# Kernel tuning notes

Measured on AMD Instinct MI355X. Metric: run time of the kernel, lower is better.

Reference implementation:

```python
import jax, jax.numpy as jnp
import numpy as np

KS = (7, 7)
ST = (3, 3)
PD = (3, 3)
DIM = 512
HID = 1960  # 40 * 49, divisible by kernel_shape


def _patch_flat_idx(out_h, out_w):
    kh, kw = KS; sh, sw = ST; ph, pw = PD
    oh = (out_h + 2 * ph - kh) // sh + 1
    ow = (out_w + 2 * pw - kw) // sw + 1
    Wp = out_w + 2 * pw
    iy = jnp.arange(kh)[:, None, None, None] + (jnp.arange(oh) * sh)[None, None, :, None]
    ix = jnp.arange(kw)[None, :, None, None] + (jnp.arange(ow) * sw)[None, None, None, :]
    # (kh, kw, oh, ow) flat index into padded image
    return (iy * Wp + ix), oh, ow


def fold(patches, out_h, out_w):
    # patches: (B, C*kh*kw, L) -> (B, C, out_h, out_w), overlap-add like F.fold
    kh, kw = KS; ph, pw = PD
    idx, oh, ow = _patch_flat_idx(out_h, out_w)
    B, CK, L = patches.shape
    C = CK // (kh * kw)
    Hp, Wp = out_h + 2 * ph, out_w + 2 * pw
    p = patches.reshape(B, C, kh, kw, oh, ow)
    out = jnp.zeros((B, C, Hp * Wp), patches.dtype)
    out = out.at[:, :, idx.reshape(-1)].add(p.reshape(B, C, -1))
    return out.reshape(B, C, Hp, Wp)[:, :, ph:ph + out_h, pw:pw + out_w]


def unfold(img, out_h, out_w):
    # img: (B, C, H, W) -> (B, C*kh*kw, L), like F.unfold
    kh, kw = KS; ph, pw = PD
    idx, oh, ow = _patch_flat_idx(out_h, out_w)
    B, C = img.shape[:2]
    imgp = jnp.pad(img, ((0, 0), (0, 0), (ph, ph), (pw, pw)))
    flat = imgp.reshape(B, C, -1)
    g = flat[:, :, idx.reshape(-1)].reshape(B, C, kh, kw, oh, ow)
    return g.reshape(B, C * kh * kw, oh * ow)


def setup_inputs() -> dict:
    key = jax.random.key(0)
    k1, k2, k3, k4, k5 = jax.random.split(key, 5)
    x = jax.random.normal(k1, (2, 5760, DIM), dtype=jnp.float32)
    W1 = jax.random.normal(k2, (HID, DIM), dtype=jnp.float32) * 0.02
    b1 = jax.random.normal(k3, (HID,), dtype=jnp.float32) * 0.02
    W2 = jax.random.normal(k4, (DIM, HID), dtype=jnp.float32) * 0.02
    b2 = jax.random.normal(k5, (DIM,), dtype=jnp.float32) * 0.02
    return {"x": x, "W1": W1, "b1": b1, "W2": W2, "b2": b2, "out_h": 60, "out_w": 108}


def reference(x, W1, b1, W2, b2, out_h, out_w):
    kh, kw = KS; sh, sw = ST; ph, pw = PD
    oh = (out_h + 2 * ph - kh) // sh + 1
    ow = (out_w + 2 * pw - kw) // sw + 1
    n_vecs = oh * ow
    h = jnp.einsum('bnd,hd->bnh', x, W1) + b1          # (b, n, HID)
    b_, n, c = h.shape
    p = h.reshape(-1, n_vecs, c).transpose(0, 2, 1)     # (B', c, L)
    folded = fold(p, out_h, out_w)                      # (B', c//49, H, W)
    ones = jnp.ones((p.shape[0], kh * kw, n_vecs), h.dtype)
    norm = fold(ones, out_h, out_w)                     # (B', 1, H, W)
    y = unfold(folded / norm, out_h, out_w)             # (B', c, L)
    y = y.transpose(0, 2, 1).reshape(b_, n, c)
    out = jnp.einsum('bnh,dh->bnd', jax.nn.gelu(y, approximate=False), W2) + b2
    return out
```

## Files before the change

### kernel.cpp

```cpp
#include <hip/hip_runtime.h>
#include <cmath>

#define M_ROWS   11520
#define DIM      512
#define HID      1960
#define HIDP     2048
#define KP2      1984
#define OH       20
#define OW       36
#define LVEC     720
#define NCH      40
#define BPRIME   16
#define HP       66
#define WP       114

typedef unsigned short u16;
typedef __bf16 bf16x8 __attribute__((ext_vector_type(8)));
typedef float  f32x4  __attribute__((ext_vector_type(4)));

__device__ __forceinline__ u16 f2bf(float f) {
    unsigned u = __float_as_uint(f);
    u += 0x7fffu + ((u >> 16) & 1u);
    return (u16)(u >> 16);
}
__device__ __forceinline__ float bf2f(u16 h) {
    return __uint_as_float(((unsigned)h) << 16);
}

__device__ __forceinline__ void gload_lds16(const void* g, void* l) {
    __builtin_amdgcn_global_load_lds(
        (const __attribute__((address_space(1))) void*)g,
        (__attribute__((address_space(3))) void*)l, 16, 0, 0);
}

#define CVT_XB   5760
#define CVT_W1B  1024
#define CVT_W2B  1024
#define CVT_Z    270
__global__ __launch_bounds__(256) void cvt_all(const float* __restrict__ x,
                                               const float* __restrict__ W1,
                                               const float* __restrict__ W2,
                                               u16* __restrict__ xb,
                                               u16* __restrict__ W1b,
                                               u16* __restrict__ W2b,
                                               u16* __restrict__ g2) {
    const int b = blockIdx.x;
    const int tid = threadIdx.x;
    ushort4 o;
    if (b < CVT_XB) {
        int i = (b * 256 + tid) * 4;
        float4 v = *(const float4*)(x + i);
        o.x = f2bf(v.x); o.y = f2bf(v.y); o.z = f2bf(v.z); o.w = f2bf(v.w);
        *(ushort4*)(xb + i) = o;
    } else if (b < CVT_XB + CVT_W1B) {
        int i = ((b - CVT_XB) * 256 + tid) * 4;
        if (i < HID * DIM) {
            float4 v = *(const float4*)(W1 + i);
            o.x = f2bf(v.x); o.y = f2bf(v.y); o.z = f2bf(v.z); o.w = f2bf(v.w);
        } else {
            o.x = o.y = o.z = o.w = 0;
        }
        *(ushort4*)(W1b + i) = o;
    } else if (b < CVT_XB + CVT_W1B + CVT_W2B) {
        int i = ((b - CVT_XB - CVT_W1B) * 256 + tid) * 4;
        int d = i / HIDP, c = i - d * HIDP;
        if (c < HID) {
            float4 v = *(const float4*)(W2 + (size_t)d * HID + c);
            o.x = f2bf(v.x); o.y = f2bf(v.y); o.z = f2bf(v.z); o.w = f2bf(v.w);
        } else {
            o.x = o.y = o.z = o.w = 0;
        }
        *(ushort4*)(W2b + i) = o;
    } else {
        int i = ((b - CVT_XB - CVT_W1B - CVT_W2B) * 256 + tid) * 4;
        int row = i / 24, c = i - row * 24;
        o.x = o.y = o.z = o.w = 0;
        *(ushort4*)(g2 + (size_t)row * HIDP + HID + c) = o;
    }
}

template <int OUT_BF16, int BN>
__global__ __launch_bounds__(512) void gemm_bt(const u16* __restrict__ A,
                                               const u16* __restrict__ B,
                                               const float* __restrict__ bias,
                                               int biasN, void* __restrict__ Cout,
                                               int N, int K, int ldk) {
    constexpr int WN = BN / 2;
    constexpr int NU = WN / 16;
    constexpr int BCH = BN * 8;

    __shared__ u16 sA[128 * 64];
    __shared__ u16 sB[BN * 64];

    const int tid  = threadIdx.x;
    const int ntn  = N / BN;
    const int NB   = gridDim.x;
    const int v    = (blockIdx.x & 7) * (NB >> 3) + (blockIdx.x >> 3);
    const int bm   = v / ntn;
    const int bn   = v - bm * ntn;
    const int lane = tid & 63;
    const int wv   = tid >> 6;
    const int wm   = (wv >> 1) * 32;
    const int wn   = (wv & 1) * WN;
    const int r    = lane & 15;
    const int quad = lane >> 4;

    const size_t Arow0 = (size_t)bm * 128 * ldk;
    const size_t Brow0 = (size_t)bn * BN * ldk;

    f32x4 acc[2][NU] = {};

    for (int kt = 0; kt < K; kt += 64) {
        __syncthreads();
#pragma unroll
        for (int i = 0; i < 2; i++) {
            int e   = i * 512 + tid;
            int row = e >> 3;
            int cp  = e & 7;
            int cg  = cp ^ (row & 7);
            gload_lds16(A + Arow0 + (size_t)row * ldk + kt + cg * 8, (char*)sA + e * 16);
        }
#pragma unroll
        for (int i = 0; i < BCH / 512; i++) {
            int e   = i * 512 + tid;
            int row = e >> 3;
            int cp  = e & 7;
            int cg  = cp ^ (row & 7);
            gload_lds16(B + Brow0 + (size_t)row * ldk + kt + cg * 8, (char*)sB + e * 16);
        }
        __syncthreads();
#pragma unroll
        for (int kk = 0; kk < 2; kk++) {
            bf16x8 af[2], bg[NU];
#pragma unroll
            for (int t = 0; t < 2; t++) {
                int row = wm + t * 16 + r;
                int c   = (kk * 4 + quad) ^ (row & 7);
                af[t] = *(const bf16x8*)(sA + row * 64 + c * 8);
            }
#pragma unroll
            for (int u = 0; u < NU; u++) {
                int row = wn + u * 16 + r;
                int c   = (kk * 4 + quad) ^ (row & 7);
                bg[u] = *(const bf16x8*)(sB + row * 64 + c * 8);
            }
#pragma unroll
            for (int t = 0; t < 2; t++)
#pragma unroll
                for (int u = 0; u < NU; u++)
                    acc[t][u] = __builtin_amdgcn_mfma_f32_16x16x32_bf16(
                        af[t], bg[u], acc[t][u], 0, 0, 0);
        }
    }

    const int gm0 = bm * 128 + wm;
    const int gn0 = bn * BN + wn;
#pragma unroll
    for (int u = 0; u < NU; u++) {
        int gn = gn0 + u * 16 + r;
        float bv = (gn < biasN) ? bias[gn] : 0.0f;
#pragma unroll
        for (int t = 0; t < 2; t++) {
            int gm = gm0 + t * 16 + quad * 4;
#pragma unroll
            for (int q = 0; q < 4; q++) {
                float v2 = acc[t][u][q] + bv;
                if (OUT_BF16)
                    ((u16*)Cout)[(size_t)(gm + q) * N + gn] = f2bf(v2);
                else
                    ((float*)Cout)[(size_t)(gm + q) * N + gn] = v2;
            }
        }
    }
}

__global__ __launch_bounds__(512) void mid_fused(const u16* __restrict__ hg,
                                                 u16* __restrict__ g2) {
    __shared__ u16 sh[12 * 20 * 56];
    __shared__ u16 sG[34 * 58];

    const int b   = blockIdx.x;
    const int bp  = b / (NCH * 4);
    const int rr  = b - bp * (NCH * 4);
    const int ch  = rr >> 2;
    const int s   = (rr >> 1) & 1;
    const int xh  = rr & 1;
    const int o0  = s * 10;
    const int lo  = s * 8;
    const int ox0 = xh * 16;
    const int n0  = bp * LVEC;
    const int c0  = ch * 49;
    const int c0f = c0 & ~7;
    const int koff = c0 & 7;
    const int tid = threadIdx.x;

    {
        const char* hb = (const char*)(hg + (size_t)(n0 + lo * 36 + ox0) * HIDP + c0f);
        for (int t = tid; t < 12 * 20 * 7; t += 512) {
            int r   = (int)(((unsigned)t * 74899u) >> 19);
            int c   = t - r * 7;
            int loy = (int)(((unsigned)r * 3277u) >> 16);
            int oxl = r - 20 * loy;
            gload_lds16(hb + (size_t)(loy * 36 + oxl) * (HIDP * 2) + c * 16,
                        (char*)sh + t * 16);
        }
    }
    __syncthreads();

    const int pxl = tid & 63;
    const int rg  = tid >> 6;
    if (pxl < 58) {
        const int  pxg  = pxl + 54 * xh;
        const bool pxin = (pxg >= 3) && (pxg <= 110);
        const int  kx0  = pxg % 3;
        int  ct[3];
        bool vx[3];
        int  cx = 0;
#pragma unroll
        for (int dx = 0; dx < 3; dx++) {
            int kx = kx0 + 3 * dx, rx = pxg - kx;
            bool ok = pxin && (kx <= 6) && (rx >= 0) && (rx <= 105);
            vx[dx] = ok;
            ct[dx] = ok ? ((rx / 3) - ox0) * 56 + kx : 0;
            cx += ok ? 1 : 0;
        }
        const float fcx = (cx == 3) ? (1.0f / 3.0f) : ((cx == 2) ? 0.5f : 1.0f);

        for (int pr = rg; pr < 34; pr += 8) {
            int py = 3 * o0 + pr;
            float val = 0.0f;
            if (pxin && py >= 3 && py <= 62) {
                int ky0 = py % 3;
                float sum = 0.0f;
                int cy = 0;
#pragma unroll
                for (int dy = 0; dy < 3; dy++) {
                    int ky = ky0 + 3 * dy, ry = py - ky;
                    if (ky <= 6 && ry >= 0 && ry <= 57) {
                        int rt = (ry / 3 - lo) * (20 * 56) + ky * 7 + koff;
                        cy++;
                        float v0 = bf2f(sh[rt + ct[0]]);
                        float v1 = bf2f(sh[rt + ct[1]]);
                        float v2 = bf2f(sh[rt + ct[2]]);
                        sum += vx[0] ? v0 : 0.0f;
                        sum += vx[1] ? v1 : 0.0f;
                        sum += vx[2] ? v2 : 0.0f;
                    }
                }
                float fcy = (cy == 3) ? (1.0f / 3.0f) : ((cy == 2) ? 0.5f : 1.0f);
                float m = sum * fcx * fcy;
                val = 0.5f * m * (1.0f + erff(m * 0.70710678118654752f));
            }
            sG[pr * 58 + pxl] = f2bf(val);
        }
    }
    __syncthreads();

    {
        u16* g2row = g2 + (size_t)(n0 + o0 * 36 + 18 * xh) * HIDP + c0;
        for (int j = tid; j < 10 * 18 * 49; j += 512) {
            int l2 = (int)(((unsigned)j * 42800u) >> 21);
            int k  = j - l2 * 49;
            int oy = (int)(((unsigned)l2 * 57u) >> 10);
            int ox = l2 - 18 * oy;
            int ky = (int)(((unsigned)k * 37u) >> 8);
            int kx = k - 7 * ky;
            g2row[(size_t)(oy * 36 + ox) * HIDP + k] =
                sG[(3 * oy + ky) * 58 + 3 * ox + kx];
        }
    }
}

extern "C" void kernel_launch(void* const* d_in, const int* in_sizes, int n_in,
                              void* d_out, int out_size, void* d_ws, size_t ws_size,
                              hipStream_t stream) {
    (void)in_sizes; (void)n_in; (void)out_size; (void)ws_size;
    const float* x  = (const float*)d_in[0];
    const float* W1 = (const float*)d_in[1];
    const float* b1 = (const float*)d_in[2];
    const float* W2 = (const float*)d_in[3];
    const float* b2 = (const float*)d_in[4];
    float* out = (float*)d_out;

    char* ws = (char*)d_ws;
    u16* xb  = (u16*)(ws);
    u16* W1b = (u16*)(ws + 11796480);
    u16* W2b = (u16*)(ws + 13893632);
    u16* hg  = (u16*)(ws + 15990784);
    u16* g2  = (u16*)(ws + 63176704);

    cvt_all<<<CVT_XB + CVT_W1B + CVT_W2B + CVT_Z, 256, 0, stream>>>(
        x, W1, W2, xb, W1b, W2b, g2);

    gemm_bt<1, 128><<<(M_ROWS / 128) * (HIDP / 128), 512, 0, stream>>>(
        xb, W1b, b1, HID, (void*)hg, HIDP, DIM, DIM);

    mid_fused<<<BPRIME * NCH * 4, 512, 0, stream>>>(hg, g2);

    gemm_bt<0, 64><<<(M_ROWS / 128) * (DIM / 64), 512, 0, stream>>>(
        g2, W2b, b2, DIM, (void*)out, DIM, KP2, HIDP);
}
```

Baseline: 186.8 us.

## Specialize GEMM kernels, use 1024-thread GEMM1 with LDS-staged coalesced output

Result: slower. 193.6 us (+3.6%).

```diff
diff --git a/kernel.cpp b/kernel.cpp
--- a/kernel.cpp
+++ b/kernel.cpp
@@ -11,12 +11,11 @@
 #define LVEC     720
 #define NCH      40
 #define BPRIME   16
-#define HP       66
-#define WP       114
 
 typedef unsigned short u16;
 typedef __bf16 bf16x8 __attribute__((ext_vector_type(8)));
 typedef float  f32x4  __attribute__((ext_vector_type(4)));
+typedef unsigned short u16x8 __attribute__((ext_vector_type(8)));
 
 __device__ __forceinline__ u16 f2bf(float f) {
     unsigned u = __float_as_uint(f);
@@ -79,97 +78,162 @@
     }
 }
 
-template <int OUT_BF16, int BN>
-__global__ __launch_bounds__(512) void gemm_bt(const u16* __restrict__ A,
-                                               const u16* __restrict__ B,
-                                               const float* __restrict__ bias,
-                                               int biasN, void* __restrict__ Cout,
-                                               int N, int K, int ldk) {
-    constexpr int WN = BN / 2;
-    constexpr int NU = WN / 16;
-    constexpr int BCH = BN * 8;
-
-    __shared__ u16 sA[128 * 64];
-    __shared__ u16 sB[BN * 64];
+__global__ __launch_bounds__(1024, 8) void gemm1_k(const u16* __restrict__ A,
+                                                   const u16* __restrict__ B,
+                                                   const float* __restrict__ bias,
+                                                   u16* __restrict__ C) {
+    __shared__ u16 smem[128 * 136];
+    u16* sA = smem;
+    u16* sB = smem + 128 * 64;
 
     const int tid  = threadIdx.x;
-    const int ntn  = N / BN;
     const int NB   = gridDim.x;
     const int v    = (blockIdx.x & 7) * (NB >> 3) + (blockIdx.x >> 3);
-    const int bm   = v / ntn;
-    const int bn   = v - bm * ntn;
+    const int bm   = v >> 4;
+    const int bn   = v & 15;
+    const int lane = tid & 63;
+    const int wv   = tid >> 6;
+    const int wm   = (wv >> 2) * 32;
+    const int wn   = (wv & 3) * 32;
+    const int r    = lane & 15;
+    const int quad = lane >> 4;
+
+    const size_t Arow0 = (size_t)bm * 128 * DIM;
+    const size_t Brow0 = (size_t)bn * 128 * DIM;
+
+    const int srow = tid >> 3;
+    const int scg  = (tid & 7) ^ (srow & 7);
+
+    f32x4 acc[2][2] = {};
+
+    for (int kt = 0; kt < DIM; kt += 64) {
+        __syncthreads();
+        gload_lds16(A + Arow0 + (size_t)srow * DIM + kt + scg * 8, (char*)sA + tid * 16);
+        gload_lds16(B + Brow0 + (size_t)srow * DIM + kt + scg * 8, (char*)sB + tid * 16);
+        __syncthreads();
+#pragma unroll
+        for (int kk = 0; kk < 2; kk++) {
+            bf16x8 af[2], bg[2];
+#pragma unroll
+            for (int m = 0; m < 2; m++) {
+                int row = wm + m * 16 + r;
+                int c   = (kk * 4 + quad) ^ (row & 7);
+                af[m] = *(const bf16x8*)(sA + row * 64 + c * 8);
+            }
+#pragma unroll
+            for (int u = 0; u < 2; u++) {
+                int row = wn + u * 16 + r;
+                int c   = (kk * 4 + quad) ^ (row & 7);
+                bg[u] = *(const bf16x8*)(sB + row * 64 + c * 8);
+            }
+#pragma unroll
+            for (int m = 0; m < 2; m++)
+#pragma unroll
+                for (int u = 0; u < 2; u++)
+                    acc[m][u] = __builtin_amdgcn_mfma_f32_16x16x32_bf16(
+                        af[m], bg[u], acc[m][u], 0, 0, 0);
+        }
+    }
+
+    __syncthreads();
+    const int gn0 = bn * 128;
+#pragma unroll
+    for (int u = 0; u < 2; u++) {
+        int gnl = wn + u * 16 + r;
+        int gng = gn0 + gnl;
+        float bv = (gng < HID) ? bias[gng] : 0.0f;
+#pragma unroll
+        for (int m = 0; m < 2; m++) {
+            int gml = wm + m * 16 + quad * 4;
+#pragma unroll
+            for (int q = 0; q < 4; q++)
+                smem[(gml + q) * 136 + gnl] = f2bf(acc[m][u][q] + bv);
+        }
+    }
+    __syncthreads();
+    const int row = tid >> 3;
+    const int seg = tid & 7;
+    const u16* src = smem + row * 136 + seg * 16;
+    u16* dst = C + (size_t)(bm * 128 + row) * HIDP + gn0 + seg * 16;
+    *(u16x8*)dst       = *(const u16x8*)src;
+    *(u16x8*)(dst + 8) = *(const u16x8*)(src + 8);
+}
+
+__global__ __launch_bounds__(512, 8) void gemm2_k(const u16* __restrict__ A,
+                                                  const u16* __restrict__ B,
+                                                  const float* __restrict__ bias,
+                                                  float* __restrict__ C) {
+    __shared__ u16 sA[128 * 64];
+    __shared__ u16 sB[64 * 64];
+
+    const int tid  = threadIdx.x;
+    const int NB   = gridDim.x;
+    const int v    = (blockIdx.x & 7) * (NB >> 3) + (blockIdx.x >> 3);
+    const int bm   = v >> 3;
+    const int bn   = v & 7;
     const int lane = tid & 63;
     const int wv   = tid >> 6;
     const int wm   = (wv >> 1) * 32;
-    const int wn   = (wv & 1) * WN;
+    const int wn   = (wv & 1) * 32;
     const int r    = lane & 15;
     const int quad = lane >> 4;
 
-    const size_t Arow0 = (size_t)bm * 128 * ldk;
-    const size_t Brow0 = (size_t)bn * BN * ldk;
-
-    f32x4 acc[2][NU] = {};
-
-    for (int kt = 0; kt < K; kt += 64) {
+    const size_t Arow0 = (size_t)bm * 128 * HIDP;
+    const size_t Brow0 = (size_t)bn * 64 * HIDP;
+
+    f32x4 acc[2][2] = {};
+
+    for (int kt = 0; kt < KP2; kt += 64) {
         __syncthreads();
 #pragma unroll
         for (int i = 0; i < 2; i++) {
             int e   = i * 512 + tid;
             int row = e >> 3;
-            int cp  = e & 7;
-            int cg  = cp ^ (row & 7);
-            gload_lds16(A + Arow0 + (size_t)row * ldk + kt + cg * 8, (char*)sA + e * 16);
-        }
-#pragma unroll
-        for (int i = 0; i < BCH / 512; i++) {
-            int e   = i * 512 + tid;
-            int row = e >> 3;
-            int cp  = e & 7;
-            int cg  = cp ^ (row & 7);
-            gload_lds16(B + Brow0 + (size_t)row * ldk + kt + cg * 8, (char*)sB + e * 16);
+            int cg  = (e & 7) ^ (row & 7);
+            gload_lds16(A + Arow0 + (size_t)row * HIDP + kt + cg * 8, (char*)sA + e * 16);
+        }
+        {
+            int row = tid >> 3;
+            int cg  = (tid & 7) ^ (row & 7);
+            gload_lds16(B + Brow0 + (size_t)row * HIDP + kt + cg * 8, (char*)sB + tid * 16);
         }
         __syncthreads();
 #pragma unroll
         for (int kk = 0; kk < 2; kk++) {
-            bf16x8 af[2], bg[NU];
-#pragma unroll
-            for (int t = 0; t < 2; t++) {
-                int row = wm + t * 16 + r;
+            bf16x8 af[2], bg[2];
+#pragma unroll
+            for (int m = 0; m < 2; m++) {
+                int row = wm + m * 16 + r;
                 int c   = (kk * 4 + quad) ^ (row & 7);
-                af[t] = *(const bf16x8*)(sA + row * 64 + c * 8);
-            }
-#pragma unroll
-            for (int u = 0; u < NU; u++) {
+                af[m] = *(const bf16x8*)(sA + row * 64 + c * 8);
+            }
+#pragma unroll
+            for (int u = 0; u < 2; u++) {
                 int row = wn + u * 16 + r;
                 int c   = (kk * 4 + quad) ^ (row & 7);
                 bg[u] = *(const bf16x8*)(sB + row * 64 + c * 8);
             }
 #pragma unroll
-            for (int t = 0; t < 2; t++)
-#pragma unroll
-                for (int u = 0; u < NU; u++)
-                    acc[t][u] = __builtin_amdgcn_mfma_f32_16x16x32_bf16(
-                        af[t], bg[u], acc[t][u], 0, 0, 0);
+            for (int m = 0; m < 2; m++)
+#pragma unroll
+                for (int u = 0; u < 2; u++)
+                    acc[m][u] = __builtin_amdgcn_mfma_f32_16x16x32_bf16(
+                        af[m], bg[u], acc[m][u], 0, 0, 0);
         }
     }
 
     const int gm0 = bm * 128 + wm;
-    const int gn0 = bn * BN + wn;
-#pragma unroll
-    for (int u = 0; u < NU; u++) {
+    const int gn0 = bn * 64 + wn;
+#pragma unroll
+    for (int u = 0; u < 2; u++) {
         int gn = gn0 + u * 16 + r;
-        float bv = (gn < biasN) ? bias[gn] : 0.0f;
-#pragma unroll
-        for (int t = 0; t < 2; t++) {
-            int gm = gm0 + t * 16 + quad * 4;
-#pragma unroll
-            for (int q = 0; q < 4; q++) {
-                float v2 = acc[t][u][q] + bv;
-                if (OUT_BF16)
-                    ((u16*)Cout)[(size_t)(gm + q) * N + gn] = f2bf(v2);
-                else
-                    ((float*)Cout)[(size_t)(gm + q) * N + gn] = v2;
-            }
+        float bv = bias[gn];
+#pragma unroll
+        for (int m = 0; m < 2; m++) {
+            int gm = gm0 + m * 16 + quad * 4;
+#pragma unroll
+            for (int q = 0; q < 4; q++)
+                C[(size_t)(gm + q) * DIM + gn] = acc[m][u][q] + bv;
         }
     }
 }
@@ -292,11 +356,9 @@
     cvt_all<<<CVT_XB + CVT_W1B + CVT_W2B + CVT_Z, 256, 0, stream>>>(
         x, W1, W2, xb, W1b, W2b, g2);
 
-    gemm_bt<1, 128><<<(M_ROWS / 128) * (HIDP / 128), 512, 0, stream>>>(
-        xb, W1b, b1, HID, (void*)hg, HIDP, DIM, DIM);
+    gemm1_k<<<(M_ROWS / 128) * (HIDP / 128), 1024, 0, stream>>>(xb, W1b, b1, hg);
 
     mid_fused<<<BPRIME * NCH * 4, 512, 0, stream>>>(hg, g2);
 
-    gemm_bt<0, 64><<<(M_ROWS / 128) * (DIM / 64), 512, 0, stream>>>(
-        g2, W2b, b2, DIM, (void*)out, DIM, KP2, HIDP);
-}
+    gemm2_k<<<(M_ROWS / 128) * (DIM / 64), 512, 0, stream>>>(g2, W2b, b2, out);
+}
```
